# Kernel tuning notes

Hardware: AMD Instinct MI355X
Metric: run time of the kernel (lower is better)

## Reference

```python
import jax, jax.numpy as jnp
import numpy as np

IMG_SIZE = 512
NUM_FREQ_MASKS = 4


def _make_masks(n, num):
    # Mirrors DCTTransform._generate_freq_masks: for i in reversed(range(num-1)),
    # an anti-triangular (low-frequency) mask of size n//2**i padded to (n,n),
    # then an all-ones mask appended last.
    masks = []
    for i in reversed(range(num - 1)):
        m = n // (2 ** i)
        tri = np.triu(np.ones((m, m), dtype=np.float32))      # upper triangular
        rot = np.rot90(tri, k=1)                               # -> i+j <= m-1 region
        pad = np.zeros((n, n), dtype=np.float32)
        pad[:m, :m] = rot
        masks.append(pad)
    masks.append(np.ones((n, n), dtype=np.float32))
    return np.stack(masks)  # [num, n, n]


def _dct_matrix(n, dtype=jnp.float32):
    # Orthonormal DCT-II matrix: X = D @ x  ==  scipy.fftpack.dct(x, axis=0, norm='ortho')
    k = jnp.arange(n, dtype=dtype)[:, None]
    m = jnp.arange(n, dtype=dtype)[None, :]
    D = jnp.cos(jnp.pi * (2.0 * m + 1.0) * k / (2.0 * n)) * jnp.sqrt(2.0 / n)
    D = D.at[0].multiply(1.0 / jnp.sqrt(2.0))  # k=0 row scale -> sqrt(1/n)
    return D


def setup_inputs() -> dict:
    key = jax.random.key(0)
    x = jax.random.normal(key, (32, 3, IMG_SIZE, IMG_SIZE), dtype=jnp.float32)
    masks = jnp.asarray(_make_masks(IMG_SIZE, NUM_FREQ_MASKS))
    return {"x": x, "masks": masks}


def reference(x, masks):
    # x: [B, C, H, W] with H == W == img_size; masks: [4, H, W]
    n = x.shape[-1]
    D = _dct_matrix(n, x.dtype)
    # 2D orthonormal DCT-II over last two axes: D @ x @ D^T (separable, order-free)
    dct2 = jnp.einsum('ij,bcjk,lk->bcil', D, x, D)
    outs = []
    for i in range(masks.shape[0]):  # small fixed loop over 4 masks
        masked = dct2 * masks[i]
        # inverse 2D DCT (IDCT-II == DCT-III, orthonormal): D^T @ y @ D
        outs.append(jnp.einsum('ji,bcjk,kl->bcil', D, masked, D))
    LH, HL, HH, LL = outs  # idx 0->LH, 1->HL, 2->HH, 3(ones)->LL per original forward
    return (LL, LH, HL, HH)
```

## Files before the change

### kernel.cpp

```cpp
#include <hip/hip_runtime.h>
#include <hip/hip_bf16.h>
#include <stdint.h>

#define NIMG 96
#define N 512
#define IMG (N*N)
#define OUT_PLANE ((long long)NIMG * IMG)

typedef __attribute__((ext_vector_type(8))) _Float16 f16x8;
typedef __attribute__((ext_vector_type(4))) float f32x4;
typedef unsigned short u16;

__device__ __forceinline__ u16 f2h(float v) {
    _Float16 h = (_Float16)v;
    return __builtin_bit_cast(u16, h);
}

__device__ __forceinline__ void gload16(const void* g, void* l) {
    __builtin_amdgcn_global_load_lds(
        (const __attribute__((address_space(1))) void*)g,
        (__attribute__((address_space(3))) void*)l, 16, 0, 0);
}

__global__ __launch_bounds__(256) void conv_x(const float* __restrict__ x,
                                              u16* __restrict__ Xcm,
                                              float* __restrict__ outLL,
                                              u16* __restrict__ Drm,
                                              u16* __restrict__ Dcm) {
    const int bid = blockIdx.x + (blockIdx.y << 4) + (blockIdx.z << 8);
    if (bid < 1024) {
        int idx = (bid << 8) + threadIdx.x;
        int k = idx >> 9, m = idx & 511;
        int r = ((2 * m + 1) * k) & 2047;
        float c = cospif((float)r * (1.0f / 1024.0f));
        float s = (k == 0) ? 0.04419417382415922f : 0.0625f;
        u16 h = f2h(c * s);
        Drm[(k << 9) + m] = h;
        Dcm[(m << 9) + k] = h;
    }

    __shared__ float t[32][33];
    const long long base = (long long)blockIdx.z * IMG;
    const int r0 = blockIdx.y * 32, c0 = blockIdx.x * 32;
    const int tr = threadIdx.x >> 3;
    const int tc = (threadIdx.x & 7) * 4;
    float4 v = *(const float4*)&x[base + (long long)(r0 + tr) * N + c0 + tc];
    *(float4*)&outLL[base + (long long)(r0 + tr) * N + c0 + tc] = v;
    t[tr][tc + 0] = v.x; t[tr][tc + 1] = v.y;
    t[tr][tc + 2] = v.z; t[tr][tc + 3] = v.w;
    __syncthreads();
    ushort4 h;
    h.x = f2h(t[tc + 0][tr]); h.y = f2h(t[tc + 1][tr]);
    h.z = f2h(t[tc + 2][tr]); h.w = f2h(t[tc + 3][tr]);
    *(ushort4*)&Xcm[base + (long long)(c0 + tr) * N + r0 + tc] = h;
}

#define GEMM_DECLS                                                         \
    const int tid = threadIdx.x;                                           \
    const int wave = tid >> 6;                                             \
    const int lane = tid & 63;                                             \
    const int srow = lane >> 2;                                            \
    const int sc8  = (lane & 3) * 8;                                       \
    const int war  = wave * 32;                                            \
    const int fr   = lane & 15;                                            \
    const int kg8  = (lane >> 4) * 8;                                      \
    const int wr   = (wave >> 1) * 64;                                     \
    const int wc   = (wave & 1) * 64;                                      \
    const int rb   = (lane >> 4) * 4;                                      \
    int aoff[4], boff[4];                                                  \
    _Pragma("unroll")                                                      \
    for (int i = 0; i < 4; ++i) {                                          \
        aoff[i] = (wr + i * 16 + fr) * 32 + kg8;                           \
        boff[i] = (wc + i * 16 + fr) * 32 + kg8;                           \
    }                                                                      \
    f32x4 acc[4][4];                                                       \
    _Pragma("unroll")                                                      \
    for (int i = 0; i < 4; ++i)                                            \
        _Pragma("unroll")                                                  \
        for (int j = 0; j < 4; ++j)                                        \
            acc[i][j] = (f32x4){0.0f, 0.0f, 0.0f, 0.0f};

#define GEMM_LOOP(Ab, lda, Bb, ldb, Keff)                                  \
    {                                                                      \
        auto stage = [&](int buf, int k0) {                                \
            _Pragma("unroll")                                              \
            for (int i = 0; i < 2; ++i) {                                  \
                int r = war + i * 16;                                      \
                gload16((Ab) + (long long)(m0 + r + srow) * (lda) + k0 + sc8, &As[buf][r * 32]); \
                gload16((Bb) + (long long)(n0 + r + srow) * (ldb) + k0 + sc8, &Bs[buf][r * 32]); \
            }                                                              \
        };                                                                 \
        auto compute = [&](int buf) {                                      \
            f16x8 af[4], bf[4];                                            \
            _Pragma("unroll")                                              \
            for (int i = 0; i < 4; ++i) af[i] = *(const f16x8*)&As[buf][aoff[i]]; \
            _Pragma("unroll")                                              \
            for (int j = 0; j < 4; ++j) bf[j] = *(const f16x8*)&Bs[buf][boff[j]]; \
            _Pragma("unroll")                                              \
            for (int i = 0; i < 4; ++i)                                    \
                _Pragma("unroll")                                          \
                for (int j = 0; j < 4; ++j)                                \
                    acc[i][j] = __builtin_amdgcn_mfma_f32_16x16x32_f16(af[i], bf[j], acc[i][j], 0, 0, 0); \
        };                                                                 \
        const int nb = (Keff) >> 5;                                        \
        stage(0, 0);                                                       \
        __syncthreads();                                                   \
        int cur = 0;                                                       \
        for (int t = 0; t < nb - 1; ++t) {                                 \
            stage(cur ^ 1, (t + 1) * 32);                                  \
            compute(cur);                                                  \
            __syncthreads();                                               \
            cur ^= 1;                                                      \
        }                                                                  \
        compute(cur);                                                      \
    }

template<int EPI>
__global__ __launch_bounds__(256, 4) void gemm16(
    const u16* __restrict__ A, long long sA, int lda,
    const u16* __restrict__ B, long long sB, int ldb,
    void* __restrict__ Cv, long long sC, int ldc,
    int K, int trilim,
    u16* __restrict__ Y2, u16* __restrict__ Y3)
{
    __shared__ u16 As[2][128 * 32];
    __shared__ u16 Bs[2][128 * 32];
    const int bz = blockIdx.z;
    int m0, n0;
    if (EPI == 3) {
        int id = blockIdx.x, ti, tj;
        if (id < 4)      { ti = 0; tj = id; }
        else if (id < 7) { ti = 1; tj = id - 4; }
        else if (id < 9) { ti = 2; tj = id - 7; }
        else             { ti = 3; tj = 0; }
        m0 = ti * 128; n0 = tj * 128;
    } else {
        m0 = blockIdx.y * 128;
        n0 = blockIdx.x * 128;
    }

    const u16* __restrict__ Ab = A + (long long)bz * sA;
    const u16* __restrict__ Bb = B + (long long)bz * sB;

    GEMM_DECLS
    GEMM_LOOP(Ab, lda, Bb, ldb, K)

    if (EPI == 1) {
        u16* Cb = (u16*)Cv + (long long)bz * sC;
        #pragma unroll
        for (int i = 0; i < 4; ++i)
            #pragma unroll
            for (int j = 0; j < 4; ++j) {
                int r = m0 + wr + i * 16 + rb;
                int c = n0 + wc + j * 16 + fr;
                #pragma unroll
                for (int g = 0; g < 4; ++g)
                    Cb[(long long)(r + g) * ldc + c] = f2h(acc[i][j][g]);
            }
    } else {
        u16* Cb = (u16*)Cv + (long long)bz * sC;
        u16* Y2b = Y2 + (long long)bz * (256 * 256);
        u16* Y3b = Y3 + (long long)bz * (128 * 128);
        const bool doY2 = (m0 + n0 < 256);
        #pragma unroll
        for (int i = 0; i < 4; ++i)
            #pragma unroll
            for (int j = 0; j < 4; ++j) {
                int r = m0 + wr + i * 16 + rb;
                int c = n0 + wc + j * 16 + fr;
                float v0 = ((r + 0) + c <= trilim) ? acc[i][j][0] : 0.0f;
                float v1 = ((r + 1) + c <= trilim) ? acc[i][j][1] : 0.0f;
                float v2 = ((r + 2) + c <= trilim) ? acc[i][j][2] : 0.0f;
                float v3 = ((r + 3) + c <= trilim) ? acc[i][j][3] : 0.0f;
                ushort4 h;
                h.x = f2h(v0); h.y = f2h(v1); h.z = f2h(v2); h.w = f2h(v3);
                *(ushort4*)&Cb[(long long)c * ldc + r] = h;
                if (doY2 && r < 256 && c < 256) {
                    ushort4 h2;
                    h2.x = ((r + 0) + c <= 255) ? h.x : (u16)0;
                    h2.y = ((r + 1) + c <= 255) ? h.y : (u16)0;
                    h2.z = ((r + 2) + c <= 255) ? h.z : (u16)0;
                    h2.w = ((r + 3) + c <= 255) ? h.w : (u16)0;
                    *(ushort4*)&Y2b[(long long)c * 256 + r] = h2;
                }
                if (r < 128 && c < 128) {
                    ushort4 h3;
                    h3.x = ((r + 0) + c <= 127) ? h.x : (u16)0;
                    h3.y = ((r + 1) + c <= 127) ? h.y : (u16)0;
                    h3.z = ((r + 2) + c <= 127) ? h.z : (u16)0;
                    h3.w = ((r + 3) + c <= 127) ? h.w : (u16)0;
                    *(ushort4*)&Y3b[(long long)c * 128 + r] = h3;
                }
            }
    }
}

__global__ __launch_bounds__(256, 4) void invA(
    const u16* __restrict__ Ycm, const u16* __restrict__ Y2,
    const u16* __restrict__ Y3, const u16* __restrict__ Dcm,
    u16* __restrict__ U, u16* __restrict__ U2, u16* __restrict__ U3)
{
    __shared__ u16 As[2][128 * 32];
    __shared__ u16 Bs[2][128 * 32];
    const int bz = blockIdx.z;
    const int id = blockIdx.x;

    const u16* __restrict__ Ab;
    u16* __restrict__ Cb;
    int lda, ldc, Keff, m0, n0;
    if (id < 16) {
        m0 = (id >> 2) * 128; n0 = (id & 3) * 128;
        Ab = Ycm + (long long)bz * IMG;     lda = 512;
        Cb = U   + (long long)bz * IMG;     ldc = 512;
        Keff = 512 - m0;
    } else if (id < 24) {
        int t = id - 16;
        m0 = (t >> 2) * 128; n0 = (t & 3) * 128;
        Ab = Y2 + (long long)bz * 65536;    lda = 256;
        Cb = U2 + (long long)bz * 131072;   ldc = 256;
        Keff = 256 - m0;
    } else {
        int t = id - 24;
        m0 = 0;              n0 = (t & 3) * 128;
        Ab = Y3 + (long long)bz * 16384;    lda = 128;
        Cb = U3 + (long long)bz * 65536;    ldc = 128;
        Keff = 128;
    }
    const u16* __restrict__ Bb = Dcm;
    const int ldb = 512;

    GEMM_DECLS
    GEMM_LOOP(Ab, lda, Bb, ldb, Keff)

    #pragma unroll
    for (int i = 0; i < 4; ++i)
        #pragma unroll
        for (int j = 0; j < 4; ++j) {
            int r = m0 + wr + i * 16 + rb;
            int c = n0 + wc + j * 16 + fr;
            ushort4 h;
            h.x = f2h(acc[i][j][0]); h.y = f2h(acc[i][j][1]);
            h.z = f2h(acc[i][j][2]); h.w = f2h(acc[i][j][3]);
            *(ushort4*)&Cb[(long long)c * ldc + r] = h;
        }
}

__global__ __launch_bounds__(256, 4) void invC(
    const u16* __restrict__ U2, const u16* __restrict__ U3,
    const u16* __restrict__ U, const u16* __restrict__ Dcm,
    float* __restrict__ outHL, float* __restrict__ outLH,
    float* __restrict__ outHH)
{
    __shared__ u16 As[2][128 * 32];
    __shared__ u16 Bs[2][128 * 32];
    const int bz = blockIdx.z;
    const int id = blockIdx.x;

    const u16* __restrict__ Ab;
    float* __restrict__ Cb;
    int lda, Keff, m0base, n0, npass;
    if (id < 16) {
        m0base = (id >> 2) * 128; n0 = (id & 3) * 128;
        Ab = U2 + (long long)bz * 131072;  lda = 256; Keff = 256;
        Cb = outHL + (long long)bz * IMG;  npass = 1;
    } else if (id < 32) {
        int t = id - 16;
        m0base = (t >> 2) * 128; n0 = (t & 3) * 128;
        Ab = U3 + (long long)bz * 65536;   lda = 128; Keff = 128;
        Cb = outLH + (long long)bz * IMG;  npass = 1;
    } else {
        int t = id - 32;
        m0base = (t >> 2) * 256; n0 = (t & 3) * 128;
        Ab = U + (long long)bz * IMG;      lda = 512; Keff = 512;
        Cb = outHH + (long long)bz * IMG;  npass = 2;
    }
    const u16* __restrict__ Bb = Dcm;
    const int ldb = 512;
    const int ldc = 512;

    for (int pass = 0; pass < npass; ++pass) {
        const int m0 = m0base + pass * 128;
        GEMM_DECLS
        GEMM_LOOP(Ab, lda, Bb, ldb, Keff)

        #pragma unroll
        for (int i = 0; i < 4; ++i)
            #pragma unroll
            for (int j = 0; j < 4; ++j) {
                int r = m0 + wr + i * 16 + rb;
                int c = n0 + wc + j * 16 + fr;
                #pragma unroll
                for (int g = 0; g < 4; ++g)
                    Cb[(long long)(r + g) * ldc + c] = acc[i][j][g];
            }
        if (pass + 1 < npass) __syncthreads();
    }
}

extern "C" void kernel_launch(void* const* d_in, const int* in_sizes, int n_in,
                              void* d_out, int out_size, void* d_ws, size_t ws_size,
                              hipStream_t stream) {
    const float* x = (const float*)d_in[0];
    float* out = (float*)d_out;
    float* outLL = out + 0 * OUT_PLANE;
    float* outLH = out + 1 * OUT_PLANE;
    float* outHL = out + 2 * OUT_PLANE;
    float* outHH = out + 3 * OUT_PLANE;

    char* ws = (char*)d_ws;
    u16* Drm = (u16*)(ws);
    u16* Dcm = (u16*)(ws + 524288);
    u16* Xcm = (u16*)(ws + 1048576);
    u16* Ycm = Xcm;
    char* reg = ws + 51380224;
    u16* T1 = (u16*)reg;
    u16* U  = (u16*)reg;
    u16* Y2 = (u16*)(ws + 101711872);
    u16* Y3 = (u16*)(ws + 114294784);
    u16* U2 = (u16*)(ws + 117440512);
    u16* U3 = (u16*)(ws + 142606336);

    const long long S = IMG;
    const int BIG = 1 << 30;

    conv_x<<<dim3(16, 16, NIMG), 256, 0, stream>>>(x, Xcm, outLL, Drm, Dcm);

    gemm16<1><<<dim3(4, 4, NIMG), 256, 0, stream>>>(
        Drm, 0, 512, Xcm, S, 512, T1, S, 512, 512, BIG, nullptr, nullptr);
    gemm16<3><<<dim3(10, 1, NIMG), 256, 0, stream>>>(
        T1, S, 512, Drm, 0, 512, Ycm, S, 512, 512, 511, Y2, Y3);
    invA<<<dim3(28, 1, NIMG), 256, 0, stream>>>(Ycm, Y2, Y3, Dcm, U, U2, U3);
    invC<<<dim3(40, 1, NIMG), 256, 0, stream>>>(U2, U3, U, Dcm, outHL, outLH, outHH);
}
```

Baseline: 322.5 us.

## Drop input transpose, reorder forward GEMMs, move LL copy into final kernel

The prep kernel now converts x to fp16 in row-major order instead of transposing it through shared memory. The first forward GEMM computes X·Dᵀ and writes its result column-major with vectorized ushort4 stores instead of scalar strided stores. The second GEMM then applies D from the left. The LL output copy of x moves out of the prep kernel into extra blocks of the final inverse kernel, so that copy runs alongside the GEMM work. The aim is to cut the transpose and scattered-store overhead; in exchange the final kernel re-reads x from memory and its grid grows.

```diff
diff --git a/kernel.cpp b/kernel.cpp
--- a/kernel.cpp
+++ b/kernel.cpp
@@ -22,12 +22,11 @@
         (__attribute__((address_space(3))) void*)l, 16, 0, 0);
 }
 
-__global__ __launch_bounds__(256) void conv_x(const float* __restrict__ x,
-                                              u16* __restrict__ Xcm,
-                                              float* __restrict__ outLL,
-                                              u16* __restrict__ Drm,
-                                              u16* __restrict__ Dcm) {
-    const int bid = blockIdx.x + (blockIdx.y << 4) + (blockIdx.z << 8);
+__global__ __launch_bounds__(256) void prep(const float* __restrict__ x,
+                                            u16* __restrict__ Xrm,
+                                            u16* __restrict__ Drm,
+                                            u16* __restrict__ Dcm) {
+    const int bid = blockIdx.x;
     if (bid < 1024) {
         int idx = (bid << 8) + threadIdx.x;
         int k = idx >> 9, m = idx & 511;
@@ -38,21 +37,11 @@
         Drm[(k << 9) + m] = h;
         Dcm[(m << 9) + k] = h;
     }
-
-    __shared__ float t[32][33];
-    const long long base = (long long)blockIdx.z * IMG;
-    const int r0 = blockIdx.y * 32, c0 = blockIdx.x * 32;
-    const int tr = threadIdx.x >> 3;
-    const int tc = (threadIdx.x & 7) * 4;
-    float4 v = *(const float4*)&x[base + (long long)(r0 + tr) * N + c0 + tc];
-    *(float4*)&outLL[base + (long long)(r0 + tr) * N + c0 + tc] = v;
-    t[tr][tc + 0] = v.x; t[tr][tc + 1] = v.y;
-    t[tr][tc + 2] = v.z; t[tr][tc + 3] = v.w;
-    __syncthreads();
+    long long idx = (long long)bid * 256 + threadIdx.x;
+    float4 v = ((const float4*)x)[idx];
     ushort4 h;
-    h.x = f2h(t[tc + 0][tr]); h.y = f2h(t[tc + 1][tr]);
-    h.z = f2h(t[tc + 2][tr]); h.w = f2h(t[tc + 3][tr]);
-    *(ushort4*)&Xcm[base + (long long)(c0 + tr) * N + r0 + tc] = h;
+    h.x = f2h(v.x); h.y = f2h(v.y); h.z = f2h(v.z); h.w = f2h(v.w);
+    ((ushort4*)Xrm)[idx] = h;
 }
 
 #define GEMM_DECLS                                                         \
@@ -145,7 +134,7 @@
     GEMM_DECLS
     GEMM_LOOP(Ab, lda, Bb, ldb, K)
 
-    if (EPI == 1) {
+    if (EPI == 2) {
         u16* Cb = (u16*)Cv + (long long)bz * sC;
         #pragma unroll
         for (int i = 0; i < 4; ++i)
@@ -153,9 +142,10 @@
             for (int j = 0; j < 4; ++j) {
                 int r = m0 + wr + i * 16 + rb;
                 int c = n0 + wc + j * 16 + fr;
-                #pragma unroll
-                for (int g = 0; g < 4; ++g)
-                    Cb[(long long)(r + g) * ldc + c] = f2h(acc[i][j][g]);
+                ushort4 h;
+                h.x = f2h(acc[i][j][0]); h.y = f2h(acc[i][j][1]);
+                h.z = f2h(acc[i][j][2]); h.w = f2h(acc[i][j][3]);
+                *(ushort4*)&Cb[(long long)c * ldc + r] = h;
             }
     } else {
         u16* Cb = (u16*)Cv + (long long)bz * sC;
@@ -248,13 +238,23 @@
 __global__ __launch_bounds__(256, 4) void invC(
     const u16* __restrict__ U2, const u16* __restrict__ U3,
     const u16* __restrict__ U, const u16* __restrict__ Dcm,
+    const float* __restrict__ x,
     float* __restrict__ outHL, float* __restrict__ outLH,
-    float* __restrict__ outHH)
+    float* __restrict__ outHH, float* __restrict__ outLL)
 {
     __shared__ u16 As[2][128 * 32];
     __shared__ u16 Bs[2][128 * 32];
     const int bz = blockIdx.z;
     const int id = blockIdx.x;
+
+    if (id >= 40) {
+        const int s = id - 40;
+        const float4* xs = (const float4*)x + (long long)bz * 65536 + s * 8192;
+        float4* ds = (float4*)outLL + (long long)bz * 65536 + s * 8192;
+        for (int t = threadIdx.x; t < 8192; t += 256)
+            ds[t] = xs[t];
+        return;
+    }
 
     const u16* __restrict__ Ab;
     float* __restrict__ Cb;
@@ -310,11 +310,11 @@
     char* ws = (char*)d_ws;
     u16* Drm = (u16*)(ws);
     u16* Dcm = (u16*)(ws + 524288);
-    u16* Xcm = (u16*)(ws + 1048576);
-    u16* Ycm = Xcm;
+    u16* Xrm = (u16*)(ws + 1048576);
+    u16* Ycm = Xrm;
     char* reg = ws + 51380224;
-    u16* T1 = (u16*)reg;
-    u16* U  = (u16*)reg;
+    u16* T2cm = (u16*)reg;
+    u16* U    = (u16*)reg;
     u16* Y2 = (u16*)(ws + 101711872);
     u16* Y3 = (u16*)(ws + 114294784);
     u16* U2 = (u16*)(ws + 117440512);
@@ -323,12 +323,13 @@
     const long long S = IMG;
     const int BIG = 1 << 30;
 
-    conv_x<<<dim3(16, 16, NIMG), 256, 0, stream>>>(x, Xcm, outLL, Drm, Dcm);
-
-    gemm16<1><<<dim3(4, 4, NIMG), 256, 0, stream>>>(
-        Drm, 0, 512, Xcm, S, 512, T1, S, 512, 512, BIG, nullptr, nullptr);
+    prep<<<dim3(24576), 256, 0, stream>>>(x, Xrm, Drm, Dcm);
+
+    gemm16<2><<<dim3(4, 4, NIMG), 256, 0, stream>>>(
+        Xrm, S, 512, Drm, 0, 512, T2cm, S, 512, 512, BIG, nullptr, nullptr);
     gemm16<3><<<dim3(10, 1, NIMG), 256, 0, stream>>>(
-        T1, S, 512, Drm, 0, 512, Ycm, S, 512, 512, 511, Y2, Y3);
+        Drm, 0, 512, T2cm, S, 512, Ycm, S, 512, 512, 511, Y2, Y3);
     invA<<<dim3(28, 1, NIMG), 256, 0, stream>>>(Ycm, Y2, Y3, Dcm, U, U2, U3);
-    invC<<<dim3(40, 1, NIMG), 256, 0, stream>>>(U2, U3, U, Dcm, outHL, outLH, outHH);
-}
+    invC<<<dim3(48, 1, NIMG), 256, 0, stream>>>(U2, U3, U, Dcm, x,
+                                                outHL, outLH, outHH, outLL);
+}
```

Result: slower. 348.9 us (+8.2%).
